# Kernel optimization log

Measured on AMD Instinct MI355X. Metric: run time of the kernel, lower is better.

Reference implementation:

```python
import jax, jax.numpy as jnp
import numpy as np
from jax.scipy.linalg import expm

DIM = 128
BF = 2          # branching_factor
H = 8           # num_heads
MAX_DEPTH = 12
PAD = BF + 1    # padding value used by pad_sequence in the torch module
N = 256         # number of positions


def setup_inputs() -> dict:
    key = jax.random.key(0)
    k1, k2 = jax.random.split(key)
    # raw _primitives parameter (the torch init applies softmax+cumsum to rand;
    # any values work for the math -- only the skew-hermitian part matters)
    prim = jax.random.uniform(k1, (BF * H + 1, DIM, DIM), dtype=jnp.float32)
    positions = jax.random.randint(k2, (N,), 0, BF ** MAX_DEPTH)  # node indices, >= 0
    return {"primitives_param": prim, "positions": positions}


def _path_words(positions):
    """Vectorized equivalent of create_paths + pad_sequence.

    For node index n the branch path is built by walking up the tree:
    branch = (n-1) % BF, parent = (n-1) // BF. Digits come out leaf->root,
    so we reverse the valid prefix and right-pad with PAD to MAX_DEPTH.
    """
    d = positions.astype(jnp.int32)
    digs = []
    for _ in range(MAX_DEPTH):
        valid = d > 0
        digs.append(jnp.where(valid, (d - 1) % BF, PAD))
        d = jnp.where(valid, (d - 1) // BF, 0)
    R = jnp.stack(digs, axis=1)            # (N, 12) leaf->root digits
    depth = jnp.sum(R != PAD, axis=1)       # path length per token
    idx = depth[:, None] - 1 - jnp.arange(MAX_DEPTH)[None, :]
    pw = jnp.take_along_axis(R, jnp.clip(idx, 0, MAX_DEPTH - 1), axis=1)
    pw = jnp.where(idx >= 0, pw, PAD)       # (N, 12) root->leaf, PAD-padded
    return pw, depth


def reference(primitives_param, positions):
    pw, depth = _path_words(positions)

    # ---- steps matrix (tree distance), mirrors the no_grad block ----
    pm = pw != PAD                                        # (N, 12)
    mask = pm[:, None, :] & pm[None, :, :]                # (N, N, 12)
    eq = pw[:, None, :] == pw[None, :, :]
    common = jnp.cumprod(eq.astype(jnp.int32), axis=-1).astype(bool) & mask
    cpl = common.sum(-1)                                  # common prefix length
    steps = depth[:, None] + depth[None, :] - 2 * cpl     # (N, N) int

    # ---- unitary primitives: expm of the skew(-hermitian, real) part ----
    skew = primitives_param - jnp.swapaxes(primitives_param, -1, -2)
    prims = expm(skew)                                    # (BF*H+1, DIM, DIM)
    sos = prims[-1]
    P = prims[:-1].reshape(BF, H, DIM, DIM)

    n_tok = pw.shape[0]
    maps = jnp.broadcast_to(jnp.eye(DIM, dtype=prims.dtype)[None, None],
                            (n_tok, H, DIM, DIM))
    sos_ptr = pw[:, 0] == -1                              # never true for pos>=0, kept for fidelity
    maps = jnp.where(sos_ptr[:, None, None, None], sos[None, None], maps)

    # fused gather-indexed scan over tree depth: instead of BF masked matmuls
    # per depth, gather each token's branch primitive and do one batched matmul.
    for d in range(MAX_DEPTH):
        sel = pw[:, d]                                    # (N,) in {0..BF-1} or PAD
        Pk = P[jnp.clip(sel, 0, BF - 1)]                  # (N, H, DIM, DIM)
        new = jnp.einsum('nhij,nhjk->nhik', maps, Pk)
        maps = jnp.where((sel < BF)[:, None, None, None], new, maps)

    return maps, steps
```

## Files before the change

### kernel.cpp

```cpp
#include <hip/hip_runtime.h>

typedef unsigned short ushort_t;
typedef unsigned int uint_t;
typedef __attribute__((ext_vector_type(8))) short bf16x8;
typedef __attribute__((ext_vector_type(4))) float f32x4;

#define NMAT 16
#define MSZ 16384

__device__ __forceinline__ ushort_t f32_bf16(float f) {
  uint_t u = __builtin_bit_cast(uint_t, f);
  u += 0x7FFFu + ((u >> 16) & 1u);
  return (ushort_t)(u >> 16);
}

__device__ __forceinline__ float bf16_f32(ushort_t b) {
  uint_t u = ((uint_t)b) << 16;
  return __builtin_bit_cast(float, u);
}

__device__ __forceinline__ int swz(int r, int k) {
  return r * 128 + (((k >> 3) ^ (r & 7)) << 3) + (k & 7);
}

__device__ __forceinline__ int tab_off(int L) {
  return (L == 1) ? 0 : (L == 2) ? 2 : (L == 3) ? 6 : 14;
}

__device__ __forceinline__ void mm_frag(const ushort_t* U, const ushort_t* V,
                                        int r0, int c0, int quad, int l16,
                                        f32x4 (&acc)[4][4]) {
#pragma unroll
  for (int rt = 0; rt < 4; rt++)
#pragma unroll
    for (int ct = 0; ct < 4; ct++) {
      f32x4 z = {0.f, 0.f, 0.f, 0.f};
      acc[rt][ct] = z;
    }
#pragma unroll
  for (int kt = 0; kt < 4; kt++) {
    int k = kt * 32 + quad * 8;
    bf16x8 a[4], b[4];
#pragma unroll
    for (int rt = 0; rt < 4; rt++) a[rt] = *(const bf16x8*)(&U[swz(r0 + rt * 16 + l16, k)]);
#pragma unroll
    for (int ct = 0; ct < 4; ct++) b[ct] = *(const bf16x8*)(&V[swz(c0 + ct * 16 + l16, k)]);
#pragma unroll
    for (int rt = 0; rt < 4; rt++)
#pragma unroll
      for (int ct = 0; ct < 4; ct++)
        acc[rt][ct] = __builtin_amdgcn_mfma_f32_16x16x32_bf16(a[rt], b[ct], acc[rt][ct], 0, 0, 0);
  }
}

__device__ __forceinline__ void store_T(ushort_t* dst, const f32x4 (&acc)[4][4],
                                        int r0, int c0, int quad, int l16,
                                        float scale, float cdiag) {
#pragma unroll
  for (int rt = 0; rt < 4; rt++)
#pragma unroll
    for (int ct = 0; ct < 4; ct++) {
      int dr = r0 + rt * 16 + quad * 4, dc = c0 + ct * 16 + l16;
      float v[4];
#pragma unroll
      for (int i = 0; i < 4; i++) {
        v[i] = scale * acc[rt][ct][i];
        if (dr + i == dc) v[i] += cdiag;
      }
      uint2 pk;
      pk.x = (uint_t)f32_bf16(v[0]) | ((uint_t)f32_bf16(v[1]) << 16);
      pk.y = (uint_t)f32_bf16(v[2]) | ((uint_t)f32_bf16(v[3]) << 16);
      *(uint2*)(&dst[swz(dc, dr)]) = pk;
    }
}

__device__ __forceinline__ void set_ident(ushort_t* dst, int t, float c) {
  ushort_t cb = f32_bf16(c);
  for (int i = 0; i < 64; i++) {
    int e = i * 256 + t;
    int r = e >> 7, k = e & 127;
    dst[swz(r, k)] = (r == k) ? cb : (ushort_t)0;
  }
}

__global__ __launch_bounds__(256, 1) void expm1_kernel(const float* __restrict__ prim,
                                                       ushort_t* __restrict__ wsCS) {
  __shared__ ushort_t __align__(16) bufA[MSZ];
  __shared__ ushort_t __align__(16) bufB[MSZ];
  int kmat = blockIdx.x >> 1, which = blockIdx.x & 1;
  int t = threadIdx.x, wave = t >> 6, lane = t & 63;
  int quad = lane >> 4, l16 = lane & 15;
  int r0 = (wave >> 1) * 64, c0 = (wave & 1) * 64;
  const float* p = prim + kmat * MSZ;

  for (int i = 0; i < 64; i++) {
    int e = i * 256 + t;
    int r = e >> 7, c = e & 127;
    bufA[swz(r, c)] = f32_bf16((p[r * 128 + c] - p[c * 128 + r]) * 0.125f);
  }
  __syncthreads();

  f32x4 acc[4][4];
  mm_frag(bufA, bufA, r0, c0, quad, l16, acc);
  __syncthreads();
  store_T(bufB, acc, r0, c0, quad, l16, -1.f, 0.f);
  __syncthreads();

  uint2 yv[4][4];
#pragma unroll
  for (int rt = 0; rt < 4; rt++)
#pragma unroll
    for (int ct = 0; ct < 4; ct++) {
      int dr = r0 + rt * 16 + quad * 4, dc = c0 + ct * 16 + l16;
      yv[rt][ct] = *(const uint2*)(&bufB[swz(dc, dr)]);
    }

  mm_frag(bufB, bufB, r0, c0, quad, l16, acc);
  __syncthreads();
  store_T(bufB, acc, r0, c0, quad, l16, 1.f, 0.f);

  float coef[9];
  if (which == 0) {
    coef[0] = 1.f; coef[1] = 1.f / 2; coef[2] = 1.f / 24; coef[3] = 1.f / 720;
    coef[4] = 1.f / 40320; coef[5] = 1.f / 3628800.f; coef[6] = 1.f / 479001600.f;
    coef[7] = 1.f / 87178291200.f; coef[8] = 1.f / 20922789888000.f;
  } else {
    coef[0] = 1.f; coef[1] = 1.f / 6; coef[2] = 1.f / 120; coef[3] = 1.f / 5040;
    coef[4] = 1.f / 362880.f; coef[5] = 1.f / 39916800.f; coef[6] = 1.f / 6227020800.f;
    coef[7] = 1.f / 1307674368000.f; coef[8] = 1.f / 355687428096000.f;
  }

  set_ident(bufA, t, coef[8]);
  __syncthreads();

#pragma unroll
  for (int k = 3; k >= 0; k--) {
    mm_frag(bufB, bufA, r0, c0, quad, l16, acc);
    __syncthreads();
    float cd = coef[2 * k], cy = coef[2 * k + 1];
#pragma unroll
    for (int rt = 0; rt < 4; rt++)
#pragma unroll
      for (int ct = 0; ct < 4; ct++) {
        int dr = r0 + rt * 16 + quad * 4, dc = c0 + ct * 16 + l16;
        uint2 yp = yv[rt][ct];
        float y[4] = {bf16_f32((ushort_t)(yp.x & 0xffff)), bf16_f32((ushort_t)(yp.x >> 16)),
                      bf16_f32((ushort_t)(yp.y & 0xffff)), bf16_f32((ushort_t)(yp.y >> 16))};
        float v[4];
#pragma unroll
        for (int i = 0; i < 4; i++) {
          v[i] = acc[rt][ct][i] + cy * y[i];
          if (dr + i == dc) v[i] += cd;
        }
        uint2 pk;
        pk.x = (uint_t)f32_bf16(v[0]) | ((uint_t)f32_bf16(v[1]) << 16);
        pk.y = (uint_t)f32_bf16(v[2]) | ((uint_t)f32_bf16(v[3]) << 16);
        *(uint2*)(&bufA[swz(dc, dr)]) = pk;
      }
    __syncthreads();
  }
  ushort_t* dst = wsCS + (size_t)(which * NMAT + kmat) * MSZ;
  for (int i = 0; i < 8; i++) {
    int e = (i * 256 + t) * 8;
    int r = e >> 7, k = e & 127;
    *(uint4*)(dst + e) = *(const uint4*)(&bufA[swz(r, k)]);
  }
}

__global__ __launch_bounds__(256, 1) void expm2_kernel(
    const float* __restrict__ prim, const ushort_t* __restrict__ wsCS,
    ushort_t* __restrict__ PN, ushort_t* __restrict__ PT) {
  __shared__ ushort_t __align__(16) bufA[MSZ];
  __shared__ ushort_t __align__(16) bufB[MSZ];
  int kmat = blockIdx.x;
  int t = threadIdx.x, wave = t >> 6, lane = t & 63;
  int quad = lane >> 4, l16 = lane & 15;
  int r0 = (wave >> 1) * 64, c0 = (wave & 1) * 64;
  const float* p = prim + kmat * MSZ;
  const ushort_t* Cg = wsCS + (size_t)kmat * MSZ;
  const ushort_t* Sg = wsCS + (size_t)(NMAT + kmat) * MSZ;

  for (int i = 0; i < 64; i++) {
    int e = i * 256 + t;
    int r = e >> 7, c = e & 127;
    bufA[swz(r, c)] = f32_bf16((p[r * 128 + c] - p[c * 128 + r]) * 0.125f);
  }
  for (int i = 0; i < 8; i++) {
    int e = (i * 256 + t) * 8;
    int r = e >> 7, k = e & 127;
    *(uint4*)(&bufB[swz(r, k)]) = *(const uint4*)(Sg + e);
  }
  __syncthreads();

  f32x4 acc[4][4];
  mm_frag(bufA, bufB, r0, c0, quad, l16, acc);
  __syncthreads();
#pragma unroll
  for (int rt = 0; rt < 4; rt++)
#pragma unroll
    for (int ct = 0; ct < 4; ct++) {
      int dr = r0 + rt * 16 + quad * 4, dc = c0 + ct * 16 + l16;
      uint2 cp = *(const uint2*)(Cg + dc * 128 + dr);
      float cf[4] = {bf16_f32((ushort_t)(cp.x & 0xffff)), bf16_f32((ushort_t)(cp.x >> 16)),
                     bf16_f32((ushort_t)(cp.y & 0xffff)), bf16_f32((ushort_t)(cp.y >> 16))};
      uint2 en, et;
      en.x = (uint_t)f32_bf16(cf[0] - acc[rt][ct][0]) | ((uint_t)f32_bf16(cf[1] - acc[rt][ct][1]) << 16);
      en.y = (uint_t)f32_bf16(cf[2] - acc[rt][ct][2]) | ((uint_t)f32_bf16(cf[3] - acc[rt][ct][3]) << 16);
      et.x = (uint_t)f32_bf16(cf[0] + acc[rt][ct][0]) | ((uint_t)f32_bf16(cf[1] + acc[rt][ct][1]) << 16);
      et.y = (uint_t)f32_bf16(cf[2] + acc[rt][ct][2]) | ((uint_t)f32_bf16(cf[3] + acc[rt][ct][3]) << 16);
      *(uint2*)(&bufA[swz(dc, dr)]) = en;
      *(uint2*)(&bufB[swz(dc, dr)]) = et;
    }
  __syncthreads();

#pragma unroll 1
  for (int sq = 0; sq < 3; sq++) {
    mm_frag(bufA, bufB, r0, c0, quad, l16, acc);
    __syncthreads();
#pragma unroll
    for (int rt = 0; rt < 4; rt++)
#pragma unroll
      for (int ct = 0; ct < 4; ct++) {
        int dr = r0 + rt * 16 + quad * 4, dc = c0 + ct * 16 + l16;
        uint2 pk;
        pk.x = (uint_t)f32_bf16(acc[rt][ct][0]) | ((uint_t)f32_bf16(acc[rt][ct][1]) << 16);
        pk.y = (uint_t)f32_bf16(acc[rt][ct][2]) | ((uint_t)f32_bf16(acc[rt][ct][3]) << 16);
        *(uint2*)(&bufB[swz(dc, dr)]) = pk;
#pragma unroll
        for (int i = 0; i < 4; i++) bufA[swz(dr + i, dc)] = f32_bf16(acc[rt][ct][i]);
      }
    __syncthreads();
  }
  for (int i = 0; i < 8; i++) {
    int e = (i * 256 + t) * 8;
    int r = e >> 7, k = e & 127;
    *(uint4*)(PN + (size_t)kmat * MSZ + e) = *(const uint4*)(&bufA[swz(r, k)]);
    *(uint4*)(PT + (size_t)kmat * MSZ + e) = *(const uint4*)(&bufB[swz(r, k)]);
  }
}

__global__ __launch_bounds__(256) void table_kernel(ushort_t* __restrict__ TN,
                                                    ushort_t* __restrict__ TT, int mode) {
  int bx = blockIdx.x;
  int eA, eB, eO, h;
  if (mode == 0) {
    int c = bx >> 3; h = bx & 7;
    eA = c >> 1; eB = c & 1; eO = 2 + c;
  } else if (bx < 64) {
    int c = bx >> 3; h = bx & 7;
    eA = 2 + (c >> 1); eB = c & 1; eO = 6 + c;
  } else {
    int c = (bx - 64) >> 3; h = (bx - 64) & 7;
    eA = 2 + (c >> 2); eB = 2 + (c & 3); eO = 14 + c;
  }
  int t = threadIdx.x, wave = t >> 6, lane = t & 63;
  int quad = lane >> 4, l16 = lane & 15;
  int r0 = (wave >> 1) * 64, c0 = (wave & 1) * 64;
  const ushort_t* A = TN + ((size_t)eA * 8 + h) * MSZ;
  const ushort_t* B = TT + ((size_t)eB * 8 + h) * MSZ;
  ushort_t* oN = TN + ((size_t)eO * 8 + h) * MSZ;
  ushort_t* oT = TT + ((size_t)eO * 8 + h) * MSZ;

  bf16x8 a[4][4], b[4][4];
#pragma unroll
  for (int kt = 0; kt < 4; kt++) {
#pragma unroll
    for (int rt = 0; rt < 4; rt++)
      a[kt][rt] = *(const bf16x8*)(A + (r0 + rt * 16 + l16) * 128 + kt * 32 + quad * 8);
#pragma unroll
    for (int ct = 0; ct < 4; ct++)
      b[kt][ct] = *(const bf16x8*)(B + (c0 + ct * 16 + l16) * 128 + kt * 32 + quad * 8);
  }
  f32x4 acc[4][4];
#pragma unroll
  for (int rt = 0; rt < 4; rt++)
#pragma unroll
    for (int ct = 0; ct < 4; ct++) {
      f32x4 z = {0.f, 0.f, 0.f, 0.f};
      acc[rt][ct] = z;
    }
#pragma unroll
  for (int kt = 0; kt < 4; kt++)
#pragma unroll
    for (int rt = 0; rt < 4; rt++)
#pragma unroll
      for (int ct = 0; ct < 4; ct++)
        acc[rt][ct] = __builtin_amdgcn_mfma_f32_16x16x32_bf16(a[kt][rt], b[kt][ct], acc[rt][ct], 0, 0, 0);
#pragma unroll
  for (int rt = 0; rt < 4; rt++)
#pragma unroll
    for (int ct = 0; ct < 4; ct++) {
      int dr = r0 + rt * 16 + quad * 4, dc = c0 + ct * 16 + l16;
      uint2 pk;
      pk.x = (uint_t)f32_bf16(acc[rt][ct][0]) | ((uint_t)f32_bf16(acc[rt][ct][1]) << 16);
      pk.y = (uint_t)f32_bf16(acc[rt][ct][2]) | ((uint_t)f32_bf16(acc[rt][ct][3]) << 16);
      *(uint2*)(oT + dc * 128 + dr) = pk;
#pragma unroll
      for (int i = 0; i < 4; i++) oN[(dr + i) * 128 + dc] = f32_bf16(acc[rt][ct][i]);
    }
}

__global__ void steps_kernel(const int* __restrict__ pos, float* __restrict__ os, int N) {
  int i = blockIdx.x, j = threadIdx.x;
  int mi = pos[i] + 1, mj = pos[j] + 1;
  int di = 31 - __builtin_clz((unsigned)mi);
  int dj = 31 - __builtin_clz((unsigned)mj);
  int tt = di < dj ? di : dj;
  unsigned x = (unsigned)((mi >> (di - tt)) ^ (mj >> (dj - tt)));
  int cpl = tt - (x ? (32 - __builtin_clz(x)) : 0);
  os[i * N + j] = (float)(di + dj - 2 * cpl);
}

__global__ __launch_bounds__(256, 2) void maps_kernel(
    const ushort_t* __restrict__ TN, const ushort_t* __restrict__ TT,
    const int* __restrict__ positions, float* __restrict__ out) {
  __shared__ ushort_t __align__(16) Mb[2][MSZ];
  int bx = blockIdx.x;
  int n = bx >> 3, h = bx & 7;
  int t = threadIdx.x, wave = t >> 6, lane = t & 63;
  int quad = lane >> 4, l16 = lane & 15;
  int m = positions[n] + 1;
  int depth = 31 - __builtin_clz((unsigned)m);
  float* ob = out + (size_t)(n * 8 + h) * MSZ;

  if (depth == 0) {
    for (int i = 0; i < 64; i++) {
      int e = i * 256 + t;
      int r = e >> 7, k = e & 127;
      ob[e] = (r == k) ? 1.0f : 0.0f;
    }
    return;
  }

  int K = (depth + 3) >> 2;
  int L0 = depth - 4 * (K - 1);
  int c0v = (m >> (depth - L0)) & ((1 << L0) - 1);
  const ushort_t* src0 = TN + ((size_t)(tab_off(L0) + c0v) * 8 + h) * MSZ;

  if (K == 1) {
    for (int i = 0; i < 8; i++) {
      int e = (i * 256 + t) * 8;
      bf16x8 v = *(const bf16x8*)(src0 + e);
#pragma unroll
      for (int j = 0; j < 8; j++) ob[e + j] = bf16_f32((ushort_t)v[j]);
    }
    return;
  }

  int r0 = (wave >> 1) * 64, c0 = (wave & 1) * 64;
#pragma unroll
  for (int i = 0; i < 8; i++) {
    int e = (i * 256 + t) * 8;
    int r = e >> 7, k = e & 127;
    *(uint4*)(&Mb[0][swz(r, k)]) = *(const uint4*)(src0 + e);
  }
  __syncthreads();

  int rem = depth - L0;
  int cur = 0;
  while (rem > 0) {
    int cb = (m >> (rem - 4)) & 15;
    const ushort_t* Ap = TT + ((size_t)(14 + cb) * 8 + h) * MSZ;
    bf16x8 a[4][4];
#pragma unroll
    for (int kt = 0; kt < 4; kt++)
#pragma unroll
      for (int rt = 0; rt < 4; rt++)
        a[kt][rt] = *(const bf16x8*)(Ap + (r0 + rt * 16 + l16) * 128 + kt * 32 + quad * 8);
    f32x4 acc[4][4];
#pragma unroll
    for (int rt = 0; rt < 4; rt++)
#pragma unroll
      for (int ct = 0; ct < 4; ct++) {
        f32x4 z = {0.f, 0.f, 0.f, 0.f};
        acc[rt][ct] = z;
      }
    const ushort_t* Lr = Mb[cur];
#pragma unroll
    for (int kt = 0; kt < 4; kt++) {
      int k = kt * 32 + quad * 8;
      bf16x8 b[4];
#pragma unroll
      for (int ct = 0; ct < 4; ct++) b[ct] = *(const bf16x8*)(&Lr[swz(c0 + ct * 16 + l16, k)]);
#pragma unroll
      for (int rt = 0; rt < 4; rt++)
#pragma unroll
        for (int ct = 0; ct < 4; ct++)
          acc[rt][ct] = __builtin_amdgcn_mfma_f32_16x16x32_bf16(a[kt][rt], b[ct], acc[rt][ct], 0, 0, 0);
    }
    rem -= 4;
    if (rem == 0) {
#pragma unroll
      for (int rt = 0; rt < 4; rt++)
#pragma unroll
        for (int ct = 0; ct < 4; ct++) {
          int dr = r0 + rt * 16 + quad * 4;
          int dc = c0 + ct * 16 + l16;
          *(f32x4*)(ob + dc * 128 + dr) = acc[rt][ct];
        }
    } else {
      ushort_t* Lw = Mb[cur ^ 1];
#pragma unroll
      for (int rt = 0; rt < 4; rt++)
#pragma unroll
        for (int ct = 0; ct < 4; ct++) {
          int dr = r0 + rt * 16 + quad * 4;
          int dc = c0 + ct * 16 + l16;
          uint2 pk;
          pk.x = (uint_t)f32_bf16(acc[rt][ct][0]) | ((uint_t)f32_bf16(acc[rt][ct][1]) << 16);
          pk.y = (uint_t)f32_bf16(acc[rt][ct][2]) | ((uint_t)f32_bf16(acc[rt][ct][3]) << 16);
          *(uint2*)(&Lw[swz(dc, dr)]) = pk;
        }
      __syncthreads();
      cur ^= 1;
    }
  }
}

extern "C" void kernel_launch(void* const* d_in, const int* in_sizes, int n_in,
                              void* d_out, int out_size, void* d_ws, size_t ws_size,
                              hipStream_t stream) {
  const float* prim = (const float*)d_in[0];
  const int* positions = (const int*)d_in[1];
  int N = in_sizes[1];
  float* out = (float*)d_out;

  ushort_t* wsCS = (ushort_t*)d_ws;
  ushort_t* TN = wsCS + (size_t)2 * NMAT * MSZ;
  ushort_t* TT = TN + (size_t)240 * MSZ;

  steps_kernel<<<N, N, 0, stream>>>(positions, out + (size_t)N * 8 * MSZ, N);
  expm1_kernel<<<2 * NMAT, 256, 0, stream>>>(prim, wsCS);
  expm2_kernel<<<NMAT, 256, 0, stream>>>(prim, wsCS, TN, TT);
  table_kernel<<<32, 256, 0, stream>>>(TN, TT, 0);
  table_kernel<<<192, 256, 0, stream>>>(TN, TT, 1);
  maps_kernel<<<(size_t)N * 8, 256, 0, stream>>>(TN, TT, positions, out);
}
```

Before: 224.3 us.

## Extend product tables to depth six and compute each map with one matmul

Precomputes branch-product tables for all prefixes up to length 6 via an extra table_kernel pass (768 blocks), so each token's map becomes at most a single 128x128 matmul of a 6-digit suffix table and a prefix table. The maps_kernel no longer loops over 4-digit chunks with LDS double buffering and barriers, and it drops the shared memory. The price is extra table-building work and workspace: 126 tables per head instead of 30. Shallow tokens now get vectorized float4 copies.

```diff
diff --git a/kernel.cpp b/kernel.cpp
--- a/kernel.cpp
+++ b/kernel.cpp
@@ -7,6 +7,7 @@
 
 #define NMAT 16
 #define MSZ 16384
+#define NTAB 126
 
 __device__ __forceinline__ ushort_t f32_bf16(float f) {
   uint_t u = __builtin_bit_cast(uint_t, f);
@@ -23,9 +24,7 @@
   return r * 128 + (((k >> 3) ^ (r & 7)) << 3) + (k & 7);
 }
 
-__device__ __forceinline__ int tab_off(int L) {
-  return (L == 1) ? 0 : (L == 2) ? 2 : (L == 3) ? 6 : 14;
-}
+__device__ __forceinline__ int tab_off(int L) { return (1 << L) - 2; }
 
 __device__ __forceinline__ void mm_frag(const ushort_t* U, const ushort_t* V,
                                         int r0, int c0, int quad, int l16,
@@ -169,7 +168,7 @@
 
 __global__ __launch_bounds__(256, 1) void expm2_kernel(
     const float* __restrict__ prim, const ushort_t* __restrict__ wsCS,
-    ushort_t* __restrict__ PN, ushort_t* __restrict__ PT) {
+    ushort_t* __restrict__ TN, ushort_t* __restrict__ TT) {
   __shared__ ushort_t __align__(16) bufA[MSZ];
   __shared__ ushort_t __align__(16) bufB[MSZ];
   int kmat = blockIdx.x;
@@ -234,8 +233,8 @@
   for (int i = 0; i < 8; i++) {
     int e = (i * 256 + t) * 8;
     int r = e >> 7, k = e & 127;
-    *(uint4*)(PN + (size_t)kmat * MSZ + e) = *(const uint4*)(&bufA[swz(r, k)]);
-    *(uint4*)(PT + (size_t)kmat * MSZ + e) = *(const uint4*)(&bufB[swz(r, k)]);
+    *(uint4*)(TN + (size_t)kmat * MSZ + e) = *(const uint4*)(&bufA[swz(r, k)]);
+    *(uint4*)(TT + (size_t)kmat * MSZ + e) = *(const uint4*)(&bufB[swz(r, k)]);
   }
 }
 
@@ -246,12 +245,22 @@
   if (mode == 0) {
     int c = bx >> 3; h = bx & 7;
     eA = c >> 1; eB = c & 1; eO = 2 + c;
-  } else if (bx < 64) {
-    int c = bx >> 3; h = bx & 7;
-    eA = 2 + (c >> 1); eB = c & 1; eO = 6 + c;
+  } else if (mode == 1) {
+    if (bx < 64) {
+      int c = bx >> 3; h = bx & 7;
+      eA = 2 + (c >> 1); eB = c & 1; eO = 6 + c;
+    } else {
+      int c = (bx - 64) >> 3; h = (bx - 64) & 7;
+      eA = 2 + (c >> 2); eB = 2 + (c & 3); eO = 14 + c;
+    }
   } else {
-    int c = (bx - 64) >> 3; h = (bx - 64) & 7;
-    eA = 2 + (c >> 2); eB = 2 + (c & 3); eO = 14 + c;
+    if (bx < 256) {
+      int c = bx >> 3; h = bx & 7;
+      eA = 2 + (c >> 3); eB = 6 + (c & 7); eO = 30 + c;
+    } else {
+      int c = (bx - 256) >> 3; h = (bx - 256) & 7;
+      eA = 6 + (c >> 3); eB = 6 + (c & 7); eO = 62 + c;
+    }
   }
   int t = threadIdx.x, wave = t >> 6, lane = t & 63;
   int quad = lane >> 4, l16 = lane & 15;
@@ -261,16 +270,6 @@
   ushort_t* oN = TN + ((size_t)eO * 8 + h) * MSZ;
   ushort_t* oT = TT + ((size_t)eO * 8 + h) * MSZ;
 
-  bf16x8 a[4][4], b[4][4];
-#pragma unroll
-  for (int kt = 0; kt < 4; kt++) {
-#pragma unroll
-    for (int rt = 0; rt < 4; rt++)
-      a[kt][rt] = *(const bf16x8*)(A + (r0 + rt * 16 + l16) * 128 + kt * 32 + quad * 8);
-#pragma unroll
-    for (int ct = 0; ct < 4; ct++)
-      b[kt][ct] = *(const bf16x8*)(B + (c0 + ct * 16 + l16) * 128 + kt * 32 + quad * 8);
-  }
   f32x4 acc[4][4];
 #pragma unroll
   for (int rt = 0; rt < 4; rt++)
@@ -280,12 +279,20 @@
       acc[rt][ct] = z;
     }
 #pragma unroll
-  for (int kt = 0; kt < 4; kt++)
+  for (int kt = 0; kt < 4; kt++) {
+    bf16x8 a[4], b[4];
+#pragma unroll
+    for (int rt = 0; rt < 4; rt++)
+      a[rt] = *(const bf16x8*)(A + (r0 + rt * 16 + l16) * 128 + kt * 32 + quad * 8);
+#pragma unroll
+    for (int ct = 0; ct < 4; ct++)
+      b[ct] = *(const bf16x8*)(B + (c0 + ct * 16 + l16) * 128 + kt * 32 + quad * 8);
 #pragma unroll
     for (int rt = 0; rt < 4; rt++)
 #pragma unroll
       for (int ct = 0; ct < 4; ct++)
-        acc[rt][ct] = __builtin_amdgcn_mfma_f32_16x16x32_bf16(a[kt][rt], b[kt][ct], acc[rt][ct], 0, 0, 0);
+        acc[rt][ct] = __builtin_amdgcn_mfma_f32_16x16x32_bf16(a[rt], b[ct], acc[rt][ct], 0, 0, 0);
+  }
 #pragma unroll
   for (int rt = 0; rt < 4; rt++)
 #pragma unroll
@@ -311,10 +318,9 @@
   os[i * N + j] = (float)(di + dj - 2 * cpl);
 }
 
-__global__ __launch_bounds__(256, 2) void maps_kernel(
+__global__ __launch_bounds__(256) void maps_kernel(
     const ushort_t* __restrict__ TN, const ushort_t* __restrict__ TT,
     const int* __restrict__ positions, float* __restrict__ out) {
-  __shared__ ushort_t __align__(16) Mb[2][MSZ];
   int bx = blockIdx.x;
   int n = bx >> 3, h = bx & 7;
   int t = threadIdx.x, wave = t >> 6, lane = t & 63;
@@ -331,90 +337,60 @@
     }
     return;
   }
-
-  int K = (depth + 3) >> 2;
-  int L0 = depth - 4 * (K - 1);
-  int c0v = (m >> (depth - L0)) & ((1 << L0) - 1);
-  const ushort_t* src0 = TN + ((size_t)(tab_off(L0) + c0v) * 8 + h) * MSZ;
-
-  if (K == 1) {
+  if (depth <= 6) {
+    int c = m & ((1 << depth) - 1);
+    const ushort_t* src = TN + ((size_t)(tab_off(depth) + c) * 8 + h) * MSZ;
     for (int i = 0; i < 8; i++) {
       int e = (i * 256 + t) * 8;
-      bf16x8 v = *(const bf16x8*)(src0 + e);
-#pragma unroll
-      for (int j = 0; j < 8; j++) ob[e + j] = bf16_f32((ushort_t)v[j]);
+      bf16x8 v = *(const bf16x8*)(src + e);
+      f32x4 lo = {bf16_f32((ushort_t)v[0]), bf16_f32((ushort_t)v[1]),
+                  bf16_f32((ushort_t)v[2]), bf16_f32((ushort_t)v[3])};
+      f32x4 hi = {bf16_f32((ushort_t)v[4]), bf16_f32((ushort_t)v[5]),
+                  bf16_f32((ushort_t)v[6]), bf16_f32((ushort_t)v[7])};
+      *(f32x4*)(ob + e) = lo;
+      *(f32x4*)(ob + e + 4) = hi;
     }
     return;
   }
 
+  int L0 = depth - 6;
+  int c0v = (m >> 6) & ((1 << L0) - 1);
+  int suf = m & 63;
+  const ushort_t* U = TT + ((size_t)(62 + suf) * 8 + h) * MSZ;
+  const ushort_t* V = TN + ((size_t)(tab_off(L0) + c0v) * 8 + h) * MSZ;
+
   int r0 = (wave >> 1) * 64, c0 = (wave & 1) * 64;
-#pragma unroll
-  for (int i = 0; i < 8; i++) {
-    int e = (i * 256 + t) * 8;
-    int r = e >> 7, k = e & 127;
-    *(uint4*)(&Mb[0][swz(r, k)]) = *(const uint4*)(src0 + e);
-  }
-  __syncthreads();
-
-  int rem = depth - L0;
-  int cur = 0;
-  while (rem > 0) {
-    int cb = (m >> (rem - 4)) & 15;
-    const ushort_t* Ap = TT + ((size_t)(14 + cb) * 8 + h) * MSZ;
-    bf16x8 a[4][4];
-#pragma unroll
-    for (int kt = 0; kt < 4; kt++)
-#pragma unroll
-      for (int rt = 0; rt < 4; rt++)
-        a[kt][rt] = *(const bf16x8*)(Ap + (r0 + rt * 16 + l16) * 128 + kt * 32 + quad * 8);
-    f32x4 acc[4][4];
-#pragma unroll
-    for (int rt = 0; rt < 4; rt++)
-#pragma unroll
-      for (int ct = 0; ct < 4; ct++) {
-        f32x4 z = {0.f, 0.f, 0.f, 0.f};
-        acc[rt][ct] = z;
-      }
-    const ushort_t* Lr = Mb[cur];
-#pragma unroll
-    for (int kt = 0; kt < 4; kt++) {
-      int k = kt * 32 + quad * 8;
-      bf16x8 b[4];
-#pragma unroll
-      for (int ct = 0; ct < 4; ct++) b[ct] = *(const bf16x8*)(&Lr[swz(c0 + ct * 16 + l16, k)]);
-#pragma unroll
-      for (int rt = 0; rt < 4; rt++)
-#pragma unroll
-        for (int ct = 0; ct < 4; ct++)
-          acc[rt][ct] = __builtin_amdgcn_mfma_f32_16x16x32_bf16(a[kt][rt], b[ct], acc[rt][ct], 0, 0, 0);
-    }
-    rem -= 4;
-    if (rem == 0) {
-#pragma unroll
-      for (int rt = 0; rt < 4; rt++)
-#pragma unroll
-        for (int ct = 0; ct < 4; ct++) {
-          int dr = r0 + rt * 16 + quad * 4;
-          int dc = c0 + ct * 16 + l16;
-          *(f32x4*)(ob + dc * 128 + dr) = acc[rt][ct];
-        }
-    } else {
-      ushort_t* Lw = Mb[cur ^ 1];
-#pragma unroll
-      for (int rt = 0; rt < 4; rt++)
-#pragma unroll
-        for (int ct = 0; ct < 4; ct++) {
-          int dr = r0 + rt * 16 + quad * 4;
-          int dc = c0 + ct * 16 + l16;
-          uint2 pk;
-          pk.x = (uint_t)f32_bf16(acc[rt][ct][0]) | ((uint_t)f32_bf16(acc[rt][ct][1]) << 16);
-          pk.y = (uint_t)f32_bf16(acc[rt][ct][2]) | ((uint_t)f32_bf16(acc[rt][ct][3]) << 16);
-          *(uint2*)(&Lw[swz(dc, dr)]) = pk;
-        }
-      __syncthreads();
-      cur ^= 1;
-    }
-  }
+  f32x4 acc[4][4];
+#pragma unroll
+  for (int rt = 0; rt < 4; rt++)
+#pragma unroll
+    for (int ct = 0; ct < 4; ct++) {
+      f32x4 z = {0.f, 0.f, 0.f, 0.f};
+      acc[rt][ct] = z;
+    }
+#pragma unroll
+  for (int kt = 0; kt < 4; kt++) {
+    bf16x8 a[4], b[4];
+#pragma unroll
+    for (int rt = 0; rt < 4; rt++)
+      a[rt] = *(const bf16x8*)(U + (r0 + rt * 16 + l16) * 128 + kt * 32 + quad * 8);
+#pragma unroll
+    for (int ct = 0; ct < 4; ct++)
+      b[ct] = *(const bf16x8*)(V + (c0 + ct * 16 + l16) * 128 + kt * 32 + quad * 8);
+#pragma unroll
+    for (int rt = 0; rt < 4; rt++)
+#pragma unroll
+      for (int ct = 0; ct < 4; ct++)
+        acc[rt][ct] = __builtin_amdgcn_mfma_f32_16x16x32_bf16(a[rt], b[ct], acc[rt][ct], 0, 0, 0);
+  }
+#pragma unroll
+  for (int rt = 0; rt < 4; rt++)
+#pragma unroll
+    for (int ct = 0; ct < 4; ct++) {
+      int dr = r0 + rt * 16 + quad * 4;
+      int dc = c0 + ct * 16 + l16;
+      *(f32x4*)(ob + dc * 128 + dr) = acc[rt][ct];
+    }
 }
 
 extern "C" void kernel_launch(void* const* d_in, const int* in_sizes, int n_in,
@@ -427,12 +403,13 @@
 
   ushort_t* wsCS = (ushort_t*)d_ws;
   ushort_t* TN = wsCS + (size_t)2 * NMAT * MSZ;
-  ushort_t* TT = TN + (size_t)240 * MSZ;
+  ushort_t* TT = TN + (size_t)NTAB * 8 * MSZ;
 
   steps_kernel<<<N, N, 0, stream>>>(positions, out + (size_t)N * 8 * MSZ, N);
   expm1_kernel<<<2 * NMAT, 256, 0, stream>>>(prim, wsCS);
   expm2_kernel<<<NMAT, 256, 0, stream>>>(prim, wsCS, TN, TT);
   table_kernel<<<32, 256, 0, stream>>>(TN, TT, 0);
   table_kernel<<<192, 256, 0, stream>>>(TN, TT, 1);
-  maps_kernel<<<(size_t)N * 8, 256, 0, stream>>>(TN, TT, positions, out);
-}
+  table_kernel<<<768, 256, 0, stream>>>(TN, TT, 2);
+  maps_kernel<<<N * 8, 256, 0, stream>>>(TN, TT, positions, out);
+}
```

Result: slower. 242.2 us (+8.0%).

## Single-buffer maps LDS, stream A fragments per k-step, raise occupancy to four

Applied to the files above, without the earlier changes.

The maps kernel drops its double-buffered shared-memory tile for a single buffer, adding an extra barrier before each in-place overwrite. It now loads the A-table fragments per k-slice instead of holding all 16 in registers. Launch bounds move from 2 to 4 blocks per CU. Together these cut LDS and register use so more blocks can run at once, hiding the global loads. The cost is an extra sync per chain step, and A loads now sit closer to the MFMAs that use them. Shallow tokens also take a vectorized float4 copy path.

```diff
diff --git a/kernel.cpp b/kernel.cpp
--- a/kernel.cpp
+++ b/kernel.cpp
@@ -7,6 +7,7 @@
 
 #define NMAT 16
 #define MSZ 16384
+#define NTAB 30
 
 __device__ __forceinline__ ushort_t f32_bf16(float f) {
   uint_t u = __builtin_bit_cast(uint_t, f);
@@ -169,7 +170,7 @@
 
 __global__ __launch_bounds__(256, 1) void expm2_kernel(
     const float* __restrict__ prim, const ushort_t* __restrict__ wsCS,
-    ushort_t* __restrict__ PN, ushort_t* __restrict__ PT) {
+    ushort_t* __restrict__ TN, ushort_t* __restrict__ TT) {
   __shared__ ushort_t __align__(16) bufA[MSZ];
   __shared__ ushort_t __align__(16) bufB[MSZ];
   int kmat = blockIdx.x;
@@ -234,8 +235,8 @@
   for (int i = 0; i < 8; i++) {
     int e = (i * 256 + t) * 8;
     int r = e >> 7, k = e & 127;
-    *(uint4*)(PN + (size_t)kmat * MSZ + e) = *(const uint4*)(&bufA[swz(r, k)]);
-    *(uint4*)(PT + (size_t)kmat * MSZ + e) = *(const uint4*)(&bufB[swz(r, k)]);
+    *(uint4*)(TN + (size_t)kmat * MSZ + e) = *(const uint4*)(&bufA[swz(r, k)]);
+    *(uint4*)(TT + (size_t)kmat * MSZ + e) = *(const uint4*)(&bufB[swz(r, k)]);
   }
 }
 
@@ -246,12 +247,14 @@
   if (mode == 0) {
     int c = bx >> 3; h = bx & 7;
     eA = c >> 1; eB = c & 1; eO = 2 + c;
-  } else if (bx < 64) {
-    int c = bx >> 3; h = bx & 7;
-    eA = 2 + (c >> 1); eB = c & 1; eO = 6 + c;
   } else {
-    int c = (bx - 64) >> 3; h = (bx - 64) & 7;
-    eA = 2 + (c >> 2); eB = 2 + (c & 3); eO = 14 + c;
+    if (bx < 64) {
+      int c = bx >> 3; h = bx & 7;
+      eA = 2 + (c >> 1); eB = c & 1; eO = 6 + c;
+    } else {
+      int c = (bx - 64) >> 3; h = (bx - 64) & 7;
+      eA = 2 + (c >> 2); eB = 2 + (c & 3); eO = 14 + c;
+    }
   }
   int t = threadIdx.x, wave = t >> 6, lane = t & 63;
   int quad = lane >> 4, l16 = lane & 15;
@@ -311,10 +314,10 @@
   os[i * N + j] = (float)(di + dj - 2 * cpl);
 }
 
-__global__ __launch_bounds__(256, 2) void maps_kernel(
+__global__ __launch_bounds__(256, 4) void maps_kernel(
     const ushort_t* __restrict__ TN, const ushort_t* __restrict__ TT,
     const int* __restrict__ positions, float* __restrict__ out) {
-  __shared__ ushort_t __align__(16) Mb[2][MSZ];
+  __shared__ ushort_t __align__(16) Mb[MSZ];
   int bx = blockIdx.x;
   int n = bx >> 3, h = bx & 7;
   int t = threadIdx.x, wave = t >> 6, lane = t & 63;
@@ -331,42 +334,40 @@
     }
     return;
   }
+  if (depth <= 4) {
+    int c = m & ((1 << depth) - 1);
+    const ushort_t* src = TN + ((size_t)(tab_off(depth) + c) * 8 + h) * MSZ;
+    for (int i = 0; i < 8; i++) {
+      int e = (i * 256 + t) * 8;
+      bf16x8 v = *(const bf16x8*)(src + e);
+      f32x4 lo = {bf16_f32((ushort_t)v[0]), bf16_f32((ushort_t)v[1]),
+                  bf16_f32((ushort_t)v[2]), bf16_f32((ushort_t)v[3])};
+      f32x4 hi = {bf16_f32((ushort_t)v[4]), bf16_f32((ushort_t)v[5]),
+                  bf16_f32((ushort_t)v[6]), bf16_f32((ushort_t)v[7])};
+      *(f32x4*)(ob + e) = lo;
+      *(f32x4*)(ob + e + 4) = hi;
+    }
+    return;
+  }
 
   int K = (depth + 3) >> 2;
   int L0 = depth - 4 * (K - 1);
   int c0v = (m >> (depth - L0)) & ((1 << L0) - 1);
   const ushort_t* src0 = TN + ((size_t)(tab_off(L0) + c0v) * 8 + h) * MSZ;
 
-  if (K == 1) {
-    for (int i = 0; i < 8; i++) {
-      int e = (i * 256 + t) * 8;
-      bf16x8 v = *(const bf16x8*)(src0 + e);
-#pragma unroll
-      for (int j = 0; j < 8; j++) ob[e + j] = bf16_f32((ushort_t)v[j]);
-    }
-    return;
-  }
-
   int r0 = (wave >> 1) * 64, c0 = (wave & 1) * 64;
 #pragma unroll
   for (int i = 0; i < 8; i++) {
     int e = (i * 256 + t) * 8;
     int r = e >> 7, k = e & 127;
-    *(uint4*)(&Mb[0][swz(r, k)]) = *(const uint4*)(src0 + e);
+    *(uint4*)(&Mb[swz(r, k)]) = *(const uint4*)(src0 + e);
   }
   __syncthreads();
 
   int rem = depth - L0;
-  int cur = 0;
   while (rem > 0) {
     int cb = (m >> (rem - 4)) & 15;
     const ushort_t* Ap = TT + ((size_t)(14 + cb) * 8 + h) * MSZ;
-    bf16x8 a[4][4];
-#pragma unroll
-    for (int kt = 0; kt < 4; kt++)
-#pragma unroll
-      for (int rt = 0; rt < 4; rt++)
-        a[kt][rt] = *(const bf16x8*)(Ap + (r0 + rt * 16 + l16) * 128 + kt * 32 + quad * 8);
     f32x4 acc[4][4];
 #pragma unroll
     for (int rt = 0; rt < 4; rt++)
@@ -375,18 +376,20 @@
         f32x4 z = {0.f, 0.f, 0.f, 0.f};
         acc[rt][ct] = z;
       }
-    const ushort_t* Lr = Mb[cur];
 #pragma unroll
     for (int kt = 0; kt < 4; kt++) {
       int k = kt * 32 + quad * 8;
-      bf16x8 b[4];
-#pragma unroll
-      for (int ct = 0; ct < 4; ct++) b[ct] = *(const bf16x8*)(&Lr[swz(c0 + ct * 16 + l16, k)]);
+      bf16x8 a[4], b[4];
 #pragma unroll
       for (int rt = 0; rt < 4; rt++)
+        a[rt] = *(const bf16x8*)(Ap + (r0 + rt * 16 + l16) * 128 + k);
+#pragma unroll
+      for (int ct = 0; ct < 4; ct++) b[ct] = *(const bf16x8*)(&Mb[swz(c0 + ct * 16 + l16, k)]);
+#pragma unroll
+      for (int rt = 0; rt < 4; rt++)
 #pragma unroll
         for (int ct = 0; ct < 4; ct++)
-          acc[rt][ct] = __builtin_amdgcn_mfma_f32_16x16x32_bf16(a[kt][rt], b[ct], acc[rt][ct], 0, 0, 0);
+          acc[rt][ct] = __builtin_amdgcn_mfma_f32_16x16x32_bf16(a[rt], b[ct], acc[rt][ct], 0, 0, 0);
     }
     rem -= 4;
     if (rem == 0) {
@@ -399,7 +402,7 @@
           *(f32x4*)(ob + dc * 128 + dr) = acc[rt][ct];
         }
     } else {
-      ushort_t* Lw = Mb[cur ^ 1];
+      __syncthreads();
 #pragma unroll
       for (int rt = 0; rt < 4; rt++)
 #pragma unroll
@@ -409,10 +412,9 @@
           uint2 pk;
           pk.x = (uint_t)f32_bf16(acc[rt][ct][0]) | ((uint_t)f32_bf16(acc[rt][ct][1]) << 16);
           pk.y = (uint_t)f32_bf16(acc[rt][ct][2]) | ((uint_t)f32_bf16(acc[rt][ct][3]) << 16);
-          *(uint2*)(&Lw[swz(dc, dr)]) = pk;
+          *(uint2*)(&Mb[swz(dc, dr)]) = pk;
         }
       __syncthreads();
-      cur ^= 1;
     }
   }
 }
@@ -427,12 +429,12 @@
 
   ushort_t* wsCS = (ushort_t*)d_ws;
   ushort_t* TN = wsCS + (size_t)2 * NMAT * MSZ;
-  ushort_t* TT = TN + (size_t)240 * MSZ;
+  ushort_t* TT = TN + (size_t)NTAB * 8 * MSZ;
 
   steps_kernel<<<N, N, 0, stream>>>(positions, out + (size_t)N * 8 * MSZ, N);
   expm1_kernel<<<2 * NMAT, 256, 0, stream>>>(prim, wsCS);
   expm2_kernel<<<NMAT, 256, 0, stream>>>(prim, wsCS, TN, TT);
   table_kernel<<<32, 256, 0, stream>>>(TN, TT, 0);
   table_kernel<<<192, 256, 0, stream>>>(TN, TT, 1);
-  maps_kernel<<<(size_t)N * 8, 256, 0, stream>>>(TN, TT, positions, out);
-}
+  maps_kernel<<<N * 8, 256, 0, stream>>>(TN, TT, positions, out);
+}
```

New measurement: 235.2 us. 1.05x slower.
